# Performance work log

Hardware: AMD Instinct MI355X
Metric: run time of the kernel (lower is better)

The kernel has to match this reference:

```python
import jax, jax.numpy as jnp
import numpy as np

B, L, D = 8, 2048, 128
CLIP_MEAN = 1.0
CLIP_STD = 10.0
U = 2.0
SMALL_LOG_STD = -10.0


def setup_inputs() -> dict:
    key = jax.random.key(0)
    ks = jax.random.split(key, 11)
    s = 1.0 / np.sqrt(D).astype(np.float32)
    inp = {
        "query": jax.random.normal(ks[0], (B, L, D), jnp.float32),
        "key": jax.random.normal(ks[1], (B, L, D), jnp.float32),
        "mask": jax.random.randint(ks[2], (B, L, L), 0, 2, jnp.int32),
        "Wq_mean": jax.random.normal(ks[3], (D, D), jnp.float32) * s,
        "bq_mean": jax.random.normal(ks[4], (D,), jnp.float32) * 0.01,
        "Wk_mean": jax.random.normal(ks[5], (D, D), jnp.float32) * s,
        "bk_mean": jax.random.normal(ks[6], (D,), jnp.float32) * 0.01,
        "Wq_std": jax.random.normal(ks[7], (D, D), jnp.float32) * s,
        "bq_std": jax.random.normal(ks[8], (D,), jnp.float32) * 0.01,
        "Wk_std": jax.random.normal(ks[9], (D, D), jnp.float32) * s,
        "bk_std": jax.random.normal(ks[10], (D,), jnp.float32) * 0.01,
    }
    return inp


def _scores(q, k):
    d_k = k.shape[-1]
    return jnp.einsum("bqd,bkd->bqk", q, k) / jnp.sqrt(jnp.asarray(d_k, q.dtype))


def reference(query, key, mask, Wq_mean, bq_mean, Wk_mean, bk_mean, Wq_std, bq_std, Wk_std, bk_std):
    # Linear projections (torch Linear: y = x @ W^T + b; here W stored as [in, out])
    qm = query @ Wq_mean + bq_mean
    km = key @ Wk_mean + bk_mean
    qs = query @ Wq_std + bq_std
    ks = key @ Wk_std + bk_std

    m = mask != 0  # [B, Lq, Lk]

    s_mean = _scores(qm, km)
    s_mean = CLIP_MEAN * (jnp.tanh(s_mean) + 1.0) * 0.5
    s_mean = jnp.where(m, s_mean, 0.0)

    s_std = _scores(qs, ks)
    s_std = (CLIP_STD - U) * ((jnp.tanh(s_std) - 1.0) * 0.5) - U
    s_std = jnp.where(m, s_std, SMALL_LOG_STD)

    return (s_mean, s_std)
```

## Files before the change

### kernel.cpp

```cpp
#include <hip/hip_runtime.h>


#define B_ 8
#define L_ 2048
#define D_ 128
#define NP (B_ * L_ * D_)
#define BLL ((size_t)B_ * L_ * L_)

typedef __attribute__((ext_vector_type(8))) short short8;
typedef __attribute__((ext_vector_type(4))) float f32x4;

__device__ __forceinline__ unsigned short f32_bf16(float x) {
  unsigned u = __float_as_uint(x);
  u += 0x7FFF + ((u >> 16) & 1);
  return (unsigned short)(u >> 16);
}
__device__ __forceinline__ float bf16_f32(unsigned short h) {
  return __uint_as_float(((unsigned)h) << 16);
}
__device__ __forceinline__ float fast_tanh(float x) {
  float e = __expf(2.0f * x);
  return 1.0f - 2.0f * __builtin_amdgcn_rcpf(e + 1.0f);
}

__global__ __launch_bounds__(256) void prep_w(
    const float* __restrict__ w0, const float* __restrict__ w1,
    const float* __restrict__ w2, const float* __restrict__ w3,
    unsigned short* __restrict__ WT) {
  int p = blockIdx.x;
  const float* W = (p == 0) ? w0 : (p == 1) ? w1 : (p == 2) ? w2 : w3;
  int idx = blockIdx.y * 256 + threadIdx.x;
  int k = idx >> 7, n = idx & 127;
  float v = W[idx];
  unsigned short h = f32_bf16(v);
  WT[p * 16384 + n * 128 + k] = h;
  WT[(4 + p) * 16384 + n * 128 + k] = f32_bf16(v - bf16_f32(h));
}

__global__ __launch_bounds__(256) void split_x(
    const float* __restrict__ q, const float* __restrict__ k,
    unsigned short* __restrict__ XS) {
  size_t idx = ((size_t)blockIdx.x * 256 + threadIdx.x) * 8;
  const float* src;
  unsigned short* dh;
  if (idx < (size_t)NP) {
    src = q + idx;
    dh = XS + idx;
  } else {
    src = k + (idx - NP);
    dh = XS + 2 * (size_t)NP + (idx - NP);
  }
  unsigned short* dl = dh + NP;
  f32x4 v0 = *(const f32x4*)src;
  f32x4 v1 = *(const f32x4*)(src + 4);
  short8 h, l;
#pragma unroll
  for (int j = 0; j < 4; j++) {
    unsigned short hh = f32_bf16(v0[j]);
    h[j] = (short)hh;
    l[j] = (short)f32_bf16(v0[j] - bf16_f32(hh));
    unsigned short hg = f32_bf16(v1[j]);
    h[4 + j] = (short)hg;
    l[4 + j] = (short)f32_bf16(v1[j] - bf16_f32(hg));
  }
  *(short8*)dh = h;
  *(short8*)dl = l;
}

__global__ __launch_bounds__(256) void proj_k(
    const unsigned short* __restrict__ XS,
    const float* __restrict__ bqm, const float* __restrict__ bkm,
    const float* __restrict__ bqs, const float* __restrict__ bks,
    const unsigned short* __restrict__ WT,
    unsigned short* __restrict__ P) {
  const int y = blockIdx.y;
  const unsigned short* Xh = XS + (size_t)y * 2 * NP;
  const unsigned short* Xl = Xh + NP;
  const float* bias_m = y ? bkm : bqm;
  const float* bias_s = y ? bks : bqs;
  const int pm = y, ps = y + 2;
  const int wave = threadIdx.x >> 6, lane = threadIdx.x & 63;
  const int lr = lane & 15, kq = lane >> 4;
  const int rowbase = blockIdx.x * 64 + wave * 16;

  const unsigned short* wmh = WT + pm * 16384;
  const unsigned short* wml = WT + (4 + pm) * 16384;
  const unsigned short* wsh = WT + ps * 16384;
  const unsigned short* wsl = WT + (4 + ps) * 16384;

  f32x4 accm[8], accs[8];
#pragma unroll
  for (int i = 0; i < 8; i++) {
    accm[i] = f32x4{0.f, 0.f, 0.f, 0.f};
    accs[i] = f32x4{0.f, 0.f, 0.f, 0.f};
  }

#pragma unroll
  for (int ks = 0; ks < 4; ks++) {
    const int koff = ks * 32 + kq * 8;
    const int ao = (rowbase + lr) * D_ + koff;
    short8 a_hi = *(const short8*)(Xh + ao);
    short8 a_lo = *(const short8*)(Xl + ao);
#pragma unroll
    for (int nt = 0; nt < 8; nt++) {
      const int wo = (nt * 16 + lr) * 128 + koff;
      short8 bh = *(const short8*)(wmh + wo);
      short8 bl = *(const short8*)(wml + wo);
      accm[nt] = __builtin_amdgcn_mfma_f32_16x16x32_bf16(a_hi, bh, accm[nt], 0, 0, 0);
      accm[nt] = __builtin_amdgcn_mfma_f32_16x16x32_bf16(a_lo, bh, accm[nt], 0, 0, 0);
      accm[nt] = __builtin_amdgcn_mfma_f32_16x16x32_bf16(a_hi, bl, accm[nt], 0, 0, 0);
      short8 ch = *(const short8*)(wsh + wo);
      short8 cl = *(const short8*)(wsl + wo);
      accs[nt] = __builtin_amdgcn_mfma_f32_16x16x32_bf16(a_hi, ch, accs[nt], 0, 0, 0);
      accs[nt] = __builtin_amdgcn_mfma_f32_16x16x32_bf16(a_lo, ch, accs[nt], 0, 0, 0);
      accs[nt] = __builtin_amdgcn_mfma_f32_16x16x32_bf16(a_hi, cl, accs[nt], 0, 0, 0);
    }
  }

  unsigned short* Pmh = P + pm * NP;
  unsigned short* Pml = P + (4 + pm) * NP;
  unsigned short* Psh = P + ps * NP;
  unsigned short* Psl = P + (4 + ps) * NP;
#pragma unroll
  for (int nt = 0; nt < 8; nt++) {
    const int col = nt * 16 + lr;
    const float bm = bias_m[col];
    const float bs = bias_s[col];
#pragma unroll
    for (int r = 0; r < 4; r++) {
      const int token = rowbase + kq * 4 + r;
      const int o = token * D_ + col;
      float vm = accm[nt][r] + bm;
      unsigned short h = f32_bf16(vm);
      Pmh[o] = h;
      Pml[o] = f32_bf16(vm - bf16_f32(h));
      float vs = accs[nt][r] + bs;
      unsigned short g = f32_bf16(vs);
      Psh[o] = g;
      Psl[o] = f32_bf16(vs - bf16_f32(g));
    }
  }
}

__global__ __launch_bounds__(256, 4) void scores_k(
    const unsigned short* __restrict__ P,
    const int* __restrict__ mask,
    float* __restrict__ out) {
  const int bid = blockIdx.x;
  const int z = bid & 7;
  const int idx = bid >> 3;
  const int q0 = (idx >> 4) * 128, c0 = (idx & 15) * 128;
  const int tid = threadIdx.x;
  const int wave = tid >> 6, lane = tid & 63;
  const int wr = wave >> 1, wc = wave & 1;
  const int lr = lane & 15, kq = lane >> 4;

  __shared__ float lt[128 * 64];

  const float rs = 0.08838834764831845f;
  unsigned long long mbits = 0ull;

  const size_t qrow = (size_t)(z * L_ + q0 + wr * 64) * D_;
  const size_t crow = (size_t)(z * L_ + c0 + wc * 64) * D_;

  for (int p = 0; p < 2; ++p) {
    const unsigned short* Qh = P + (size_t)(2 * p) * NP + qrow;
    const unsigned short* Ql = Qh + 4 * (size_t)NP;
    const unsigned short* Kh = P + (size_t)(2 * p + 1) * NP + crow;
    const unsigned short* Kl = Kh + 4 * (size_t)NP;

    f32x4 acc[4][4];
#pragma unroll
    for (int i = 0; i < 4; i++)
#pragma unroll
      for (int j = 0; j < 4; j++) acc[i][j] = f32x4{0.f, 0.f, 0.f, 0.f};

#pragma unroll
    for (int ks = 0; ks < 4; ks++) {
      const int koff = ks * 32 + kq * 8;
      short8 qh[4], ql[4];
#pragma unroll
      for (int t = 0; t < 4; t++) {
        const int ro = (t * 16 + lr) * D_ + koff;
        qh[t] = *(const short8*)(Qh + ro);
        ql[t] = *(const short8*)(Ql + ro);
      }
#pragma unroll
      for (int ni = 0; ni < 4; ni++) {
        const int ro = (ni * 16 + lr) * D_ + koff;
        short8 kh = *(const short8*)(Kh + ro);
        short8 kl = *(const short8*)(Kl + ro);
#pragma unroll
        for (int mi = 0; mi < 4; mi++) {
          acc[mi][ni] = __builtin_amdgcn_mfma_f32_16x16x32_bf16(qh[mi], kh, acc[mi][ni], 0, 0, 0);
          acc[mi][ni] = __builtin_amdgcn_mfma_f32_16x16x32_bf16(ql[mi], kh, acc[mi][ni], 0, 0, 0);
          acc[mi][ni] = __builtin_amdgcn_mfma_f32_16x16x32_bf16(qh[mi], kl, acc[mi][ni], 0, 0, 0);
        }
      }
    }

    for (int chunk = 0; chunk < 2; ++chunk) {
      if (wc == chunk) {
#pragma unroll
        for (int mi = 0; mi < 4; mi++)
#pragma unroll
          for (int r = 0; r < 4; r++) {
            const int row = wr * 64 + mi * 16 + kq * 4 + r;
            const int xr = ((row >> 2) & 3) << 4;
#pragma unroll
            for (int ni = 0; ni < 4; ni++)
              lt[row * 64 + ((ni * 16 + lr) ^ xr)] = acc[mi][ni][r];
          }
      }
      __syncthreads();
#pragma unroll
      for (int it = 0; it < 8; ++it) {
        const int di = it * 256 + tid;
        const int row = di >> 4;
        const int c4 = (di & 15) * 4;
        const int xr = ((row >> 2) & 3) << 4;
        f32x4 v = *(const f32x4*)&lt[row * 64 + (c4 ^ xr)];
        const size_t a = ((size_t)(z * L_ + q0 + row)) * L_ + c0 + chunk * 64 + c4;
        const int bbase = chunk * 32 + it * 4;
        f32x4 o;
        if (p == 0) {
          const int4 m4 = *(const int4*)&mask[a];
          const int mv[4] = {m4.x, m4.y, m4.z, m4.w};
#pragma unroll
          for (int j = 0; j < 4; j++) {
            float t = fast_tanh(v[j] * rs);
            o[j] = mv[j] ? (0.5f * t + 0.5f) : 0.0f;
            if (mv[j]) mbits |= (1ull << (bbase + j));
          }
          *(f32x4*)&out[a] = o;
        } else {
#pragma unroll
          for (int j = 0; j < 4; j++) {
            float t = fast_tanh(v[j] * rs);
            const bool mv = (mbits >> (bbase + j)) & 1ull;
            o[j] = mv ? (4.0f * t - 6.0f) : -10.0f;
          }
          *(f32x4*)&out[BLL + a] = o;
        }
      }
      __syncthreads();
    }
  }
}

extern "C" void kernel_launch(void* const* d_in, const int* in_sizes, int n_in,
                              void* d_out, int out_size, void* d_ws, size_t ws_size,
                              hipStream_t stream) {
  const float* query = (const float*)d_in[0];
  const float* key   = (const float*)d_in[1];
  const int*   mask  = (const int*)d_in[2];
  const float* Wqm   = (const float*)d_in[3];
  const float* bqm   = (const float*)d_in[4];
  const float* Wkm   = (const float*)d_in[5];
  const float* bkm   = (const float*)d_in[6];
  const float* Wqs   = (const float*)d_in[7];
  const float* bqs   = (const float*)d_in[8];
  const float* Wks   = (const float*)d_in[9];
  const float* bks   = (const float*)d_in[10];

  unsigned short* P  = (unsigned short*)d_ws;
  unsigned short* WT = P + 8 * (size_t)NP;
  unsigned short* XS = WT + 8 * 16384;

  prep_w<<<dim3(4, 64), 256, 0, stream>>>(Wqm, Wkm, Wqs, Wks, WT);
  split_x<<<dim3(2048), 256, 0, stream>>>(query, key, XS);
  proj_k<<<dim3(256, 2), 256, 0, stream>>>(XS, bqm, bkm, bqs, bks, WT, P);
  scores_k<<<dim3(2048), 256, 0, stream>>>(P, mask, (float*)d_out);
}
```

Before: 614.4 us.

## Restructure scores kernel into 16-row strips computing mean and std together

Each block now handles 16 query rows across all 2048 key columns in chunks of 256, computing the mean and std score tiles in the same pass instead of two sequential passes over 128x128 tiles. It drops the K low-part correction term, going from 3-term to 2-term bf16 split products, which reduces MFMA work and K loads at some accuracy cost. Mask loads and output stores use nontemporal hints, and the grid is halved to 1024 blocks. The smaller M tile means K data is reloaded per 16-row strip, which raises global/L2 read traffic, and there are more barriers per block.

Result: faster. 596.7 us (-2.9%).

```diff
diff --git a/kernel.cpp b/kernel.cpp
--- a/kernel.cpp
+++ b/kernel.cpp
@@ -9,6 +9,7 @@
 
 typedef __attribute__((ext_vector_type(8))) short short8;
 typedef __attribute__((ext_vector_type(4))) float f32x4;
+typedef __attribute__((ext_vector_type(4))) int i32x4;
 
 __device__ __forceinline__ unsigned short f32_bf16(float x) {
   unsigned u = __float_as_uint(x);
@@ -148,103 +149,111 @@
     float* __restrict__ out) {
   const int bid = blockIdx.x;
   const int z = bid & 7;
-  const int idx = bid >> 3;
-  const int q0 = (idx >> 4) * 128, c0 = (idx & 15) * 128;
+  const int q0 = (bid >> 3) * 16;
   const int tid = threadIdx.x;
   const int wave = tid >> 6, lane = tid & 63;
-  const int wr = wave >> 1, wc = wave & 1;
   const int lr = lane & 15, kq = lane >> 4;
 
-  __shared__ float lt[128 * 64];
+  __shared__ float tb[16 * 256];
 
   const float rs = 0.08838834764831845f;
-  unsigned long long mbits = 0ull;
-
-  const size_t qrow = (size_t)(z * L_ + q0 + wr * 64) * D_;
-  const size_t crow = (size_t)(z * L_ + c0 + wc * 64) * D_;
-
-  for (int p = 0; p < 2; ++p) {
-    const unsigned short* Qh = P + (size_t)(2 * p) * NP + qrow;
-    const unsigned short* Ql = Qh + 4 * (size_t)NP;
-    const unsigned short* Kh = P + (size_t)(2 * p + 1) * NP + crow;
-    const unsigned short* Kl = Kh + 4 * (size_t)NP;
-
-    f32x4 acc[4][4];
-#pragma unroll
-    for (int i = 0; i < 4; i++)
-#pragma unroll
-      for (int j = 0; j < 4; j++) acc[i][j] = f32x4{0.f, 0.f, 0.f, 0.f};
+
+  const size_t qbase = (size_t)(z * L_ + q0) * D_;
+  const size_t kbase = (size_t)(z * L_) * D_;
+  const unsigned short* Qmh = P + 0 * (size_t)NP + qbase;
+  const unsigned short* Qml = P + 4 * (size_t)NP + qbase;
+  const unsigned short* Qsh = P + 2 * (size_t)NP + qbase;
+  const unsigned short* Qsl = P + 6 * (size_t)NP + qbase;
+  const unsigned short* Kmh = P + 1 * (size_t)NP + kbase;
+  const unsigned short* Ksh = P + 3 * (size_t)NP + kbase;
+
+  for (int cc = 0; cc < 8; ++cc) {
+    const int colb = cc * 256 + wave * 64;
+
+    f32x4 am[4], as_[4];
+#pragma unroll
+    for (int i = 0; i < 4; i++) {
+      am[i] = f32x4{0.f, 0.f, 0.f, 0.f};
+      as_[i] = f32x4{0.f, 0.f, 0.f, 0.f};
+    }
 
 #pragma unroll
     for (int ks = 0; ks < 4; ks++) {
-      const int koff = ks * 32 + kq * 8;
-      short8 qh[4], ql[4];
-#pragma unroll
-      for (int t = 0; t < 4; t++) {
-        const int ro = (t * 16 + lr) * D_ + koff;
-        qh[t] = *(const short8*)(Qh + ro);
-        ql[t] = *(const short8*)(Ql + ro);
-      }
+      const int ko = ks * 32 + kq * 8;
+      const int ao = lr * D_ + ko;
+      short8 qmh = *(const short8*)(Qmh + ao);
+      short8 qml = *(const short8*)(Qml + ao);
+      short8 qsh = *(const short8*)(Qsh + ao);
+      short8 qsl = *(const short8*)(Qsl + ao);
 #pragma unroll
       for (int ni = 0; ni < 4; ni++) {
-        const int ro = (ni * 16 + lr) * D_ + koff;
-        short8 kh = *(const short8*)(Kh + ro);
-        short8 kl = *(const short8*)(Kl + ro);
-#pragma unroll
-        for (int mi = 0; mi < 4; mi++) {
-          acc[mi][ni] = __builtin_amdgcn_mfma_f32_16x16x32_bf16(qh[mi], kh, acc[mi][ni], 0, 0, 0);
-          acc[mi][ni] = __builtin_amdgcn_mfma_f32_16x16x32_bf16(ql[mi], kh, acc[mi][ni], 0, 0, 0);
-          acc[mi][ni] = __builtin_amdgcn_mfma_f32_16x16x32_bf16(qh[mi], kl, acc[mi][ni], 0, 0, 0);
-        }
-      }
-    }
-
-    for (int chunk = 0; chunk < 2; ++chunk) {
-      if (wc == chunk) {
-#pragma unroll
-        for (int mi = 0; mi < 4; mi++)
-#pragma unroll
-          for (int r = 0; r < 4; r++) {
-            const int row = wr * 64 + mi * 16 + kq * 4 + r;
-            const int xr = ((row >> 2) & 3) << 4;
-#pragma unroll
-            for (int ni = 0; ni < 4; ni++)
-              lt[row * 64 + ((ni * 16 + lr) ^ xr)] = acc[mi][ni][r];
-          }
-      }
-      __syncthreads();
-#pragma unroll
-      for (int it = 0; it < 8; ++it) {
-        const int di = it * 256 + tid;
-        const int row = di >> 4;
-        const int c4 = (di & 15) * 4;
-        const int xr = ((row >> 2) & 3) << 4;
-        f32x4 v = *(const f32x4*)&lt[row * 64 + (c4 ^ xr)];
-        const size_t a = ((size_t)(z * L_ + q0 + row)) * L_ + c0 + chunk * 64 + c4;
-        const int bbase = chunk * 32 + it * 4;
-        f32x4 o;
-        if (p == 0) {
-          const int4 m4 = *(const int4*)&mask[a];
-          const int mv[4] = {m4.x, m4.y, m4.z, m4.w};
-#pragma unroll
-          for (int j = 0; j < 4; j++) {
-            float t = fast_tanh(v[j] * rs);
-            o[j] = mv[j] ? (0.5f * t + 0.5f) : 0.0f;
-            if (mv[j]) mbits |= (1ull << (bbase + j));
-          }
-          *(f32x4*)&out[a] = o;
-        } else {
-#pragma unroll
-          for (int j = 0; j < 4; j++) {
-            float t = fast_tanh(v[j] * rs);
-            const bool mv = (mbits >> (bbase + j)) & 1ull;
-            o[j] = mv ? (4.0f * t - 6.0f) : -10.0f;
-          }
-          *(f32x4*)&out[BLL + a] = o;
-        }
-      }
-      __syncthreads();
-    }
+        const int ro = (colb + ni * 16 + lr) * D_ + ko;
+        short8 bm = *(const short8*)(Kmh + ro);
+        short8 bs = *(const short8*)(Ksh + ro);
+        am[ni] = __builtin_amdgcn_mfma_f32_16x16x32_bf16(qmh, bm, am[ni], 0, 0, 0);
+        am[ni] = __builtin_amdgcn_mfma_f32_16x16x32_bf16(qml, bm, am[ni], 0, 0, 0);
+        as_[ni] = __builtin_amdgcn_mfma_f32_16x16x32_bf16(qsh, bs, as_[ni], 0, 0, 0);
+        as_[ni] = __builtin_amdgcn_mfma_f32_16x16x32_bf16(qsl, bs, as_[ni], 0, 0, 0);
+      }
+    }
+
+#pragma unroll
+    for (int ni = 0; ni < 4; ni++)
+#pragma unroll
+      for (int r = 0; r < 4; r++) {
+        const int row = kq * 4 + r;
+        const int col = wave * 64 + ni * 16 + lr;
+        tb[row * 256 + (col ^ (kq << 4))] = am[ni][r];
+      }
+    __syncthreads();
+
+    unsigned mb = 0;
+#pragma unroll
+    for (int it = 0; it < 4; ++it) {
+      const int idx = it * 256 + tid;
+      const int row = idx >> 6;
+      const int c4 = (idx & 63) * 4;
+      f32x4 v = *(const f32x4*)&tb[row * 256 + (c4 ^ ((row >> 2) << 4))];
+      const size_t a = ((size_t)(z * L_ + q0 + row)) * L_ + cc * 256 + c4;
+      i32x4 m4 = __builtin_nontemporal_load((const i32x4*)&mask[a]);
+      f32x4 o;
+#pragma unroll
+      for (int j = 0; j < 4; j++) {
+        float t = fast_tanh(v[j] * rs);
+        o[j] = m4[j] ? (0.5f * t + 0.5f) : 0.0f;
+        if (m4[j]) mb |= (1u << (it * 4 + j));
+      }
+      __builtin_nontemporal_store(o, (f32x4*)&out[a]);
+    }
+    __syncthreads();
+
+#pragma unroll
+    for (int ni = 0; ni < 4; ni++)
+#pragma unroll
+      for (int r = 0; r < 4; r++) {
+        const int row = kq * 4 + r;
+        const int col = wave * 64 + ni * 16 + lr;
+        tb[row * 256 + (col ^ (kq << 4))] = as_[ni][r];
+      }
+    __syncthreads();
+
+#pragma unroll
+    for (int it = 0; it < 4; ++it) {
+      const int idx = it * 256 + tid;
+      const int row = idx >> 6;
+      const int c4 = (idx & 63) * 4;
+      f32x4 v = *(const f32x4*)&tb[row * 256 + (c4 ^ ((row >> 2) << 4))];
+      const size_t a = ((size_t)(z * L_ + q0 + row)) * L_ + cc * 256 + c4;
+      f32x4 o;
+#pragma unroll
+      for (int j = 0; j < 4; j++) {
+        float t = fast_tanh(v[j] * rs);
+        const bool mv = (mb >> (it * 4 + j)) & 1u;
+        o[j] = mv ? (4.0f * t - 6.0f) : -10.0f;
+      }
+      __builtin_nontemporal_store(o, (f32x4*)&out[BLL + a]);
+    }
+    __syncthreads();
   }
 }
 
@@ -270,5 +279,5 @@
   prep_w<<<dim3(4, 64), 256, 0, stream>>>(Wqm, Wkm, Wqs, Wks, WT);
   split_x<<<dim3(2048), 256, 0, stream>>>(query, key, XS);
   proj_k<<<dim3(256, 2), 256, 0, stream>>>(XS, bqm, bkm, bqs, bks, WT, P);
-  scores_k<<<dim3(2048), 256, 0, stream>>>(P, mask, (float*)d_out);
-}
+  scores_k<<<dim3(1024), 256, 0, stream>>>(P, mask, (float*)d_out);
+}
```
